# Performance work log

Hardware: AMD Instinct MI355X
Metric: run time of the kernel (lower is better)

Reference implementation:

```python
import jax, jax.numpy as jnp
import numpy as np

N = 100000   # nodes
E = 1600000  # edges
F = 128      # num_features
NF = 4       # n_factor
D = 64       # n_dim = dim // n_factor = 256 // 4
NL = 3       # n_layer
G = 128      # num graphs in batch


def setup_inputs() -> dict:
    key = jax.random.key(0)
    ks = jax.random.split(key, 10)
    s = 0.05
    x = jax.random.normal(ks[0], (N, F), jnp.float32)
    edge_index = jax.random.randint(ks[1], (2, E), 0, N)
    att = jax.random.uniform(ks[2], (NF, E), jnp.float32)
    batch = jnp.sort(jax.random.randint(ks[3], (N,), 0, G))
    lin_W = jax.random.normal(ks[4], (NF, F, D), jnp.float32) * s
    lin_b = jnp.zeros((NF, D), jnp.float32)
    conv_Wrel = jax.random.normal(ks[5], (NF, NL, D, D), jnp.float32) * s
    conv_brel = jnp.zeros((NF, NL, D), jnp.float32)
    conv_Wroot = jax.random.normal(ks[6], (NF, NL, D, D), jnp.float32) * s
    gru_Wih = jax.random.normal(ks[7], (NF, 3 * D, D), jnp.float32) * s
    gru_Whh = jax.random.normal(ks[8], (NF, 3 * D, D), jnp.float32) * s
    gru_bih = jnp.zeros((NF, 3 * D), jnp.float32)
    gru_bhh = jnp.zeros((NF, 3 * D), jnp.float32)
    return dict(x=x, edge_index=edge_index, att=att, batch=batch,
                lin_W=lin_W, lin_b=lin_b,
                conv_Wrel=conv_Wrel, conv_brel=conv_brel, conv_Wroot=conv_Wroot,
                gru_Wih=gru_Wih, gru_Whh=gru_Whh, gru_bih=gru_bih, gru_bhh=gru_bhh,
                num_graphs=G)


def _gru_cell(xin, h, Wih, Whh, bih, bhh):
    # torch.nn.GRU single step: r,z,n gates
    gi = xin @ Wih.T + bih  # [N, 3D]
    gh = h @ Whh.T + bhh
    ir, iz, inn = jnp.split(gi, 3, axis=-1)
    hr, hz, hn = jnp.split(gh, 3, axis=-1)
    r = jax.nn.sigmoid(ir + hr)
    z = jax.nn.sigmoid(iz + hz)
    n = jnp.tanh(inn + r * hn)
    return (1.0 - z) * n + z * h


def reference(x, edge_index, att, batch, lin_W, lin_b, conv_Wrel, conv_brel,
              conv_Wroot, gru_Wih, gru_Whh, gru_bih, gru_bhh, num_graphs):
    src, dst = edge_index[0], edge_index[1]
    counts = jax.ops.segment_sum(jnp.ones((N,), x.dtype), batch, num_segments=num_graphs)
    counts = jnp.maximum(counts, 1.0)[:, None]
    outs, feats = [], []
    for f in range(NF):
        w = att[f][:, None]                       # [E,1] edge weights for this factor
        out = x @ lin_W[f] + lin_b[f]             # [N,D]
        h = out                                   # initial GRU hidden state
        for l in range(NL):
            # GraphConv: lin_rel(scatter_add(w * x_src -> dst)) + lin_root(x)
            agg = jax.ops.segment_sum(out[src] * w, dst, num_segments=N)
            m = jax.nn.relu(agg @ conv_Wrel[f, l] + conv_brel[f, l] + out @ conv_Wroot[f, l])
            h = _gru_cell(m, h, gru_Wih[f], gru_Whh[f], gru_bih[f], gru_bhh[f])
            out = h
        feats.append(out)
        # global mean pool
        outs.append(jax.ops.segment_sum(out, batch, num_segments=num_graphs) / counts)
    return (jnp.stack(outs), jnp.stack(feats))
```

## Files before the change

kernel.cpp:

```cpp
#include <hip/hip_runtime.h>

#define NN   100000
#define EE   1600000
#define FDIM 128
#define NFAC 4
#define DD   64
#define NLAY 3
#define GG   128
#define ROW  (NFAC * DD)

#define PF_STRIDE 57344
#define OFF_WREL  8192
#define OFF_WROOT 20480
#define OFF_WIH   32768
#define OFF_WHH   45056
#define PREP_TOTAL (NFAC * PF_STRIDE)

typedef __bf16 bf16x8_t __attribute__((ext_vector_type(8)));
typedef float  f32x4_t  __attribute__((ext_vector_type(4)));

__device__ __forceinline__ unsigned short f2bf(float x) {
    unsigned u = __float_as_uint(x);
    u += 0x7fffu + ((u >> 16) & 1u);
    return (unsigned short)(u >> 16);
}
__device__ __forceinline__ float b2f(unsigned short h) {
    return __uint_as_float(((unsigned)h) << 16);
}
__device__ __forceinline__ float sigm(float x) { return 1.f / (1.f + __expf(-x)); }
__device__ __forceinline__ float tanh_f(float x) {
    float t = __expf(-2.f * fabsf(x));
    float r = (1.f - t) / (1.f + t);
    return x >= 0.f ? r : -r;
}

__global__ __launch_bounds__(256) void k_init(int* deg, int* cursor, float* outs) {
    int i = blockIdx.x * 256 + threadIdx.x;
    if (i < NN) { deg[i] = 0; cursor[i] = 0; }
    if (i < NFAC * GG * DD) outs[i] = 0.f;
}

__global__ __launch_bounds__(256) void k_prep(const float* x, const float* linW,
                                              const float* wrel, const float* wroot,
                                              const float* wih, const float* whh,
                                              unsigned short* x16, unsigned short* prep) {
    for (int i = blockIdx.x * 256 + threadIdx.x; i < NN * FDIM; i += gridDim.x * 256)
        x16[i] = f2bf(x[i]);
    for (int idx = blockIdx.x * 256 + threadIdx.x; idx < PREP_TOTAL; idx += gridDim.x * 256) {
        int f = idx / PF_STRIDE, r = idx % PF_STRIDE;
        int e, KB, mode, l = 0;
        if (r < OFF_WREL)       { e = r;                 KB = 4; mode = 0; }
        else if (r < OFF_WROOT) { int rr = r - OFF_WREL;  l = rr >> 12; e = rr & 4095; KB = 2; mode = 1; }
        else if (r < OFF_WIH)   { int rr = r - OFF_WROOT; l = rr >> 12; e = rr & 4095; KB = 2; mode = 2; }
        else if (r < OFF_WHH)   { e = r - OFF_WIH;        KB = 2; mode = 3; }
        else                    { e = r - OFF_WHH;        KB = 2; mode = 4; }
        int j = e & 7, lane = (e >> 3) & 63, t = e >> 9;
        int kb = t % KB, nt = t / KB;
        int k = kb * 32 + (lane >> 4) * 8 + j;
        int n = nt * 16 + (lane & 15);
        float v;
        if (mode == 0)      v = linW[(f * FDIM + k) * DD + n];
        else if (mode == 1) v = wrel[((f * 3 + l) * DD + k) * DD + n];
        else if (mode == 2) v = wroot[((f * 3 + l) * DD + k) * DD + n];
        else if (mode == 3) v = wih[(f * 192 + n) * DD + k];
        else                v = whh[(f * 192 + n) * DD + k];
        prep[idx] = f2bf(v);
    }
}

__global__ __launch_bounds__(256) void k_count(const int* batch, float* counts) {
    __shared__ int lb[GG + 1];
    int t = threadIdx.x;
    if (t <= GG) {
        int lo = 0, hi = NN;
        while (lo < hi) { int mid = (lo + hi) >> 1; if (batch[mid] < t) lo = mid + 1; else hi = mid; }
        lb[t] = lo;
    }
    __syncthreads();
    if (t < GG) counts[t] = (float)(lb[t + 1] - lb[t]);
}

__global__ __launch_bounds__(256) void k_deg(const int* ei, int* deg) {
    int e = blockIdx.x * 256 + threadIdx.x;
    if (e < EE) atomicAdd(&deg[ei[EE + e]], 1);
}
__global__ __launch_bounds__(256) void k_scan1(const int* deg, int* row_pos, int* bsum) {
    __shared__ int lds[256];
    int tid = threadIdx.x, idx = blockIdx.x * 256 + tid;
    int v = (idx < NN) ? deg[idx] : 0;
    lds[tid] = v; __syncthreads();
    for (int s = 1; s < 256; s <<= 1) {
        int t = (tid >= s) ? lds[tid - s] : 0;
        __syncthreads();
        lds[tid] += t;
        __syncthreads();
    }
    if (idx < NN) row_pos[idx] = lds[tid] - v;
    if (tid == 255) bsum[blockIdx.x] = lds[255];
}
__global__ __launch_bounds__(512) void k_scan2(int* bsum) {
    __shared__ int lds[512];
    int tid = threadIdx.x;
    int v = (tid < 391) ? bsum[tid] : 0;
    lds[tid] = v; __syncthreads();
    for (int s = 1; s < 512; s <<= 1) {
        int t = (tid >= s) ? lds[tid - s] : 0;
        __syncthreads();
        lds[tid] += t;
        __syncthreads();
    }
    bsum[tid] = lds[tid] - v;
}
__global__ __launch_bounds__(256) void k_rowptr(const int* row_pos, const int* boff, int* row_ptr) {
    int i = blockIdx.x * 256 + threadIdx.x;
    if (i < NN) row_ptr[i] = row_pos[i] + boff[i >> 8];
    if (i == 0) row_ptr[NN] = EE;
}
__global__ __launch_bounds__(256) void k_fill(const int* ei, const float* att,
                                              const int* row_ptr, int* cursor,
                                              int* csr_src, float* csr_att) {
    int e = blockIdx.x * 256 + threadIdx.x;
    if (e >= EE) return;
    int d = ei[EE + e];
    int slot = row_ptr[d] + atomicAdd(&cursor[d], 1);
    csr_src[slot] = ei[e];
    *(float4*)(csr_att + (size_t)slot * 4) =
        make_float4(att[e], att[EE + e], att[2 * EE + e], att[3 * EE + e]);
}

__global__ __launch_bounds__(256) void k_lin(const unsigned short* x16, const unsigned short* prep,
                                             const float* linb, unsigned short* out16) {
    int f = blockIdx.y, n0 = blockIdx.x * 64;
    __shared__ unsigned short xs[64 * 136];
    int tid = threadIdx.x;
    for (int t = tid; t < 1024; t += 256) {
        int row = t >> 4, seg = t & 15;
        int gn = n0 + row; if (gn >= NN) gn = NN - 1;
        *(uint4*)(xs + row * 136 + seg * 8) = *(const uint4*)(x16 + gn * FDIM + seg * 8);
    }
    __syncthreads();
    int w = tid >> 6, lane = tid & 63, mrow = lane & 15, q = lane >> 4;
    const unsigned short* wp = prep + f * PF_STRIDE;
#pragma unroll
    for (int nt = 0; nt < 4; nt++) {
        f32x4_t acc = {0.f, 0.f, 0.f, 0.f};
#pragma unroll
        for (int kb = 0; kb < 4; kb++) {
            bf16x8_t a = *(const bf16x8_t*)(xs + (w * 16 + mrow) * 136 + kb * 32 + q * 8);
            bf16x8_t b = *(const bf16x8_t*)(wp + ((nt * 4 + kb) * 64 + lane) * 8);
            acc = __builtin_amdgcn_mfma_f32_16x16x32_bf16(a, b, acc, 0, 0, 0);
        }
        int col = nt * 16 + mrow;
        float bias = linb[f * DD + col];
#pragma unroll
        for (int r = 0; r < 4; r++) {
            int node = n0 + w * 16 + q * 4 + r;
            if (node < NN) out16[(size_t)node * ROW + f * DD + col] = f2bf(acc[r] + bias);
        }
    }
}

__global__ __launch_bounds__(256) void k_gather(const int* row_ptr, const int* csr_src, const float* csr_att,
                                                const unsigned short* out16, unsigned short* agg16) {
    int wave = threadIdx.x >> 6, lane = threadIdx.x & 63;
    int n = blockIdx.x * 4 + wave;
    if (n >= NN) return;
    int row = row_ptr[n], end = row_ptr[n + 1];
    int total = end - row;
    int fsel = lane >> 4, loff = lane * 4;
    float a0 = 0.f, a1 = 0.f, a2 = 0.f, a3 = 0.f;
    for (int base = 0; base < total; base += 8) {
        int s[8]; float w[8];
#pragma unroll
        for (int j = 0; j < 8; j++) {
            int e = base + j;
            int idx = row + (e < total ? e : total - 1);
            s[j] = csr_src[idx];
            float ww = csr_att[(size_t)idx * 4 + fsel];
            w[j] = (e < total) ? ww : 0.f;
        }
        uint2 v[8];
#pragma unroll
        for (int j = 0; j < 8; j++)
            v[j] = *(const uint2*)(out16 + (size_t)s[j] * ROW + loff);
#pragma unroll
        for (int j = 0; j < 8; j++) {
            a0 = fmaf(w[j], __uint_as_float(v[j].x << 16), a0);
            a1 = fmaf(w[j], __uint_as_float(v[j].x & 0xffff0000u), a1);
            a2 = fmaf(w[j], __uint_as_float(v[j].y << 16), a2);
            a3 = fmaf(w[j], __uint_as_float(v[j].y & 0xffff0000u), a3);
        }
    }
    ushort4 r;
    r.x = f2bf(a0); r.y = f2bf(a1); r.z = f2bf(a2); r.w = f2bf(a3);
    *(ushort4*)(agg16 + (size_t)n * ROW + loff) = r;
}

__global__ __launch_bounds__(256) void k_layer(int l, const unsigned short* agg16, unsigned short* out16,
                                               const unsigned short* prep, const float* brel,
                                               const float* bih, const float* bhh,
                                               float* feats, int last) {
    int f = blockIdx.y, n0 = blockIdx.x * 64;
    __shared__ unsigned short A1[64 * 72];
    __shared__ unsigned short A2[64 * 72];
    __shared__ unsigned short Mt[64 * 72];
    int tid = threadIdx.x;
    for (int t = tid; t < 512; t += 256) {
        int row = t >> 3, seg = t & 7;
        int gn = n0 + row; if (gn >= NN) gn = NN - 1;
        *(uint4*)(A1 + row * 72 + seg * 8) = *(const uint4*)(agg16 + (size_t)gn * ROW + f * DD + seg * 8);
        *(uint4*)(A2 + row * 72 + seg * 8) = *(const uint4*)(out16 + (size_t)gn * ROW + f * DD + seg * 8);
    }
    __syncthreads();
    int w = tid >> 6, lane = tid & 63, mrow = lane & 15, q = lane >> 4;
    const unsigned short* wrel  = prep + f * PF_STRIDE + OFF_WREL  + l * 4096;
    const unsigned short* wroot = prep + f * PF_STRIDE + OFF_WROOT + l * 4096;

#pragma unroll
    for (int nt = 0; nt < 4; nt++) {
        f32x4_t acc = {0.f, 0.f, 0.f, 0.f};
#pragma unroll
        for (int kb = 0; kb < 2; kb++) {
            bf16x8_t a1 = *(const bf16x8_t*)(A1 + (w * 16 + mrow) * 72 + kb * 32 + q * 8);
            bf16x8_t b1 = *(const bf16x8_t*)(wrel + ((nt * 2 + kb) * 64 + lane) * 8);
            acc = __builtin_amdgcn_mfma_f32_16x16x32_bf16(a1, b1, acc, 0, 0, 0);
            bf16x8_t a2 = *(const bf16x8_t*)(A2 + (w * 16 + mrow) * 72 + kb * 32 + q * 8);
            bf16x8_t b2 = *(const bf16x8_t*)(wroot + ((nt * 2 + kb) * 64 + lane) * 8);
            acc = __builtin_amdgcn_mfma_f32_16x16x32_bf16(a2, b2, acc, 0, 0, 0);
        }
        int col = nt * 16 + mrow;
        float bias = brel[(f * 3 + l) * DD + col];
#pragma unroll
        for (int r = 0; r < 4; r++) {
            float mv = acc[r] + bias;
            mv = mv > 0.f ? mv : 0.f;
            Mt[(w * 16 + q * 4 + r) * 72 + col] = f2bf(mv);
        }
    }
    __syncthreads();

    const unsigned short* wih = prep + f * PF_STRIDE + OFF_WIH;
    const unsigned short* whh = prep + f * PF_STRIDE + OFF_WHH;
#pragma unroll
    for (int nt = 0; nt < 4; nt++) {
        f32x4_t ir = {0.f,0.f,0.f,0.f}, iz = {0.f,0.f,0.f,0.f}, in_ = {0.f,0.f,0.f,0.f};
        f32x4_t hr = {0.f,0.f,0.f,0.f}, hz = {0.f,0.f,0.f,0.f}, hn  = {0.f,0.f,0.f,0.f};
#pragma unroll
        for (int kb = 0; kb < 2; kb++) {
            bf16x8_t am = *(const bf16x8_t*)(Mt + (w * 16 + mrow) * 72 + kb * 32 + q * 8);
            bf16x8_t ah = *(const bf16x8_t*)(A2 + (w * 16 + mrow) * 72 + kb * 32 + q * 8);
            bf16x8_t br = *(const bf16x8_t*)(wih + (((nt)     * 2 + kb) * 64 + lane) * 8);
            bf16x8_t bz = *(const bf16x8_t*)(wih + (((nt + 4) * 2 + kb) * 64 + lane) * 8);
            bf16x8_t bn = *(const bf16x8_t*)(wih + (((nt + 8) * 2 + kb) * 64 + lane) * 8);
            ir = __builtin_amdgcn_mfma_f32_16x16x32_bf16(am, br, ir, 0, 0, 0);
            iz = __builtin_amdgcn_mfma_f32_16x16x32_bf16(am, bz, iz, 0, 0, 0);
            in_ = __builtin_amdgcn_mfma_f32_16x16x32_bf16(am, bn, in_, 0, 0, 0);
            bf16x8_t cr = *(const bf16x8_t*)(whh + (((nt)     * 2 + kb) * 64 + lane) * 8);
            bf16x8_t cz = *(const bf16x8_t*)(whh + (((nt + 4) * 2 + kb) * 64 + lane) * 8);
            bf16x8_t cn = *(const bf16x8_t*)(whh + (((nt + 8) * 2 + kb) * 64 + lane) * 8);
            hr = __builtin_amdgcn_mfma_f32_16x16x32_bf16(ah, cr, hr, 0, 0, 0);
            hz = __builtin_amdgcn_mfma_f32_16x16x32_bf16(ah, cz, hz, 0, 0, 0);
            hn = __builtin_amdgcn_mfma_f32_16x16x32_bf16(ah, cn, hn, 0, 0, 0);
        }
        int col = nt * 16 + mrow;
        float bi_r = bih[f * 192 + col],        bh_r = bhh[f * 192 + col];
        float bi_z = bih[f * 192 + 64 + col],   bh_z = bhh[f * 192 + 64 + col];
        float bi_n = bih[f * 192 + 128 + col],  bh_n = bhh[f * 192 + 128 + col];
#pragma unroll
        for (int r = 0; r < 4; r++) {
            float rg = sigm(ir[r] + bi_r + hr[r] + bh_r);
            float z  = sigm(iz[r] + bi_z + hz[r] + bh_z);
            float nn = tanh_f(in_[r] + bi_n + rg * (hn[r] + bh_n));
            float h  = b2f(A2[(w * 16 + q * 4 + r) * 72 + col]);
            float hp = (1.f - z) * nn + z * h;
            int node = n0 + w * 16 + q * 4 + r;
            if (node < NN) {
                out16[(size_t)node * ROW + f * DD + col] = f2bf(hp);
                if (last) feats[((size_t)f * NN + node) * DD + col] = hp;
            }
        }
    }
}

__global__ __launch_bounds__(256) void k_pool(const float* feats, const int* batch, float* outs) {
    int f = blockIdx.y, w = threadIdx.x >> 6, lane = threadIdx.x & 63;
    int nbase = blockIdx.x * 256 + w * 64;
    if (nbase >= NN) return;
    int g_cur = batch[nbase];
    float acc = 0.f;
    for (int i = 0; i < 64; i++) {
        int n = nbase + i;
        if (n >= NN) break;
        int g = batch[n];
        float v = feats[((size_t)f * NN + n) * DD + lane];
        if (g != g_cur) {
            atomicAdd(&outs[(f * GG + g_cur) * DD + lane], acc);
            acc = v; g_cur = g;
        } else acc += v;
    }
    atomicAdd(&outs[(f * GG + g_cur) * DD + lane], acc);
}
__global__ __launch_bounds__(256) void k_norm(float* outs, const float* counts) {
    int i = blockIdx.x * 256 + threadIdx.x;
    if (i < NFAC * GG * DD) {
        int g = (i >> 6) & (GG - 1);
        outs[i] /= fmaxf(counts[g], 1.f);
    }
}

extern "C" void kernel_launch(void* const* d_in, const int* in_sizes, int n_in,
                              void* d_out, int out_size, void* d_ws, size_t ws_size,
                              hipStream_t stream) {
    const float* x    = (const float*)d_in[0];
    const int*   ei   = (const int*)d_in[1];
    const float* att  = (const float*)d_in[2];
    const int*   batch= (const int*)d_in[3];
    const float* linW = (const float*)d_in[4];
    const float* linb = (const float*)d_in[5];
    const float* wrel = (const float*)d_in[6];
    const float* brel = (const float*)d_in[7];
    const float* wroot= (const float*)d_in[8];
    const float* wih  = (const float*)d_in[9];
    const float* whh  = (const float*)d_in[10];
    const float* bih  = (const float*)d_in[11];
    const float* bhh  = (const float*)d_in[12];

    float* outs  = (float*)d_out;
    float* feats = (float*)d_out + NFAC * GG * DD;

    char* p = (char*)d_ws;
    unsigned short* out16 = (unsigned short*)p; p += (size_t)NN * ROW * 2;
    unsigned short* agg16 = (unsigned short*)p; p += (size_t)NN * ROW * 2;
    unsigned short* x16   = (unsigned short*)p; p += (size_t)NN * FDIM * 2;
    unsigned short* prep  = (unsigned short*)p; p += (size_t)PREP_TOTAL * 2;
    float* csr_att        = (float*)p;          p += (size_t)EE * 16;
    int* csr_src          = (int*)p;            p += (size_t)EE * 4;
    int* deg              = (int*)p;            p += (size_t)NN * 4;
    int* cursor           = (int*)p;            p += (size_t)NN * 4;
    int* row_pos          = (int*)p;            p += (size_t)NN * 4;
    int* row_ptr          = (int*)p;            p += (size_t)(NN + 1) * 4;
    int* boff             = (int*)p;            p += 512 * 4;
    float* counts         = (float*)p;          p += 512;

    k_init  <<<dim3(391),  dim3(256), 0, stream>>>(deg, cursor, outs);
    k_prep  <<<dim3(4096), dim3(256), 0, stream>>>(x, linW, wrel, wroot, wih, whh, x16, prep);
    k_count <<<dim3(1),    dim3(256), 0, stream>>>(batch, counts);
    k_deg   <<<dim3(6250), dim3(256), 0, stream>>>(ei, deg);
    k_scan1 <<<dim3(391),  dim3(256), 0, stream>>>(deg, row_pos, boff);
    k_scan2 <<<dim3(1),    dim3(512), 0, stream>>>(boff);
    k_rowptr<<<dim3(391),  dim3(256), 0, stream>>>(row_pos, boff, row_ptr);
    k_fill  <<<dim3(6250), dim3(256), 0, stream>>>(ei, att, row_ptr, cursor, csr_src, csr_att);
    k_lin   <<<dim3(1563, 4), dim3(256), 0, stream>>>(x16, prep, linb, out16);
    for (int l = 0; l < NLAY; l++) {
        k_gather<<<dim3(25000),   dim3(256), 0, stream>>>(row_ptr, csr_src, csr_att, out16, agg16);
        k_layer <<<dim3(1563, 4), dim3(256), 0, stream>>>(l, agg16, out16, prep, brel, bih, bhh,
                                                          feats, (l == NLAY - 1) ? 1 : 0);
    }
    k_pool <<<dim3(391, 4), dim3(256), 0, stream>>>(feats, batch, outs);
    k_norm <<<dim3(128),    dim3(256), 0, stream>>>(outs, counts);
}
```

Baseline: 1.050 ms.

## Fuse edge gather with conv+GRU layer kernel and ping-pong hidden buffers

The separate gather and layer kernels are merged into one kernel per layer. Each 64-node block gathers neighbor aggregates for all four factors into shared memory and then runs the conv and GRU MFMAs, with one wave assigned per factor. This removes the agg16 round trip through global memory and one launch per layer, and double-buffers the hidden state so the in-place update is not read by other blocks mid-layer. In exchange, the gather now has much less parallelism (1563 blocks with 16 serial nodes per wave instead of 25000 blocks), and the larger shared-memory footprint limits occupancy, which may expose latency.

```diff
diff --git a/kernel.cpp b/kernel.cpp
--- a/kernel.cpp
+++ b/kernel.cpp
@@ -15,6 +15,8 @@
 #define OFF_WIH   32768
 #define OFF_WHH   45056
 #define PREP_TOTAL (NFAC * PF_STRIDE)
+
+#define LPAD 264
 
 typedef __bf16 bf16x8_t __attribute__((ext_vector_type(8)));
 typedef float  f32x4_t  __attribute__((ext_vector_type(4)));
@@ -130,153 +132,180 @@
 
 __global__ __launch_bounds__(256) void k_lin(const unsigned short* x16, const unsigned short* prep,
                                              const float* linb, unsigned short* out16) {
-    int f = blockIdx.y, n0 = blockIdx.x * 64;
+    int n0 = blockIdx.x * 64;
     __shared__ unsigned short xs[64 * 136];
     int tid = threadIdx.x;
     for (int t = tid; t < 1024; t += 256) {
         int row = t >> 4, seg = t & 15;
         int gn = n0 + row; if (gn >= NN) gn = NN - 1;
-        *(uint4*)(xs + row * 136 + seg * 8) = *(const uint4*)(x16 + gn * FDIM + seg * 8);
+        *(uint4*)(xs + row * 136 + seg * 8) = *(const uint4*)(x16 + (size_t)gn * FDIM + seg * 8);
     }
     __syncthreads();
     int w = tid >> 6, lane = tid & 63, mrow = lane & 15, q = lane >> 4;
-    const unsigned short* wp = prep + f * PF_STRIDE;
-#pragma unroll
-    for (int nt = 0; nt < 4; nt++) {
-        f32x4_t acc = {0.f, 0.f, 0.f, 0.f};
-#pragma unroll
-        for (int kb = 0; kb < 4; kb++) {
-            bf16x8_t a = *(const bf16x8_t*)(xs + (w * 16 + mrow) * 136 + kb * 32 + q * 8);
-            bf16x8_t b = *(const bf16x8_t*)(wp + ((nt * 4 + kb) * 64 + lane) * 8);
-            acc = __builtin_amdgcn_mfma_f32_16x16x32_bf16(a, b, acc, 0, 0, 0);
-        }
-        int col = nt * 16 + mrow;
-        float bias = linb[f * DD + col];
-#pragma unroll
-        for (int r = 0; r < 4; r++) {
-            int node = n0 + w * 16 + q * 4 + r;
-            if (node < NN) out16[(size_t)node * ROW + f * DD + col] = f2bf(acc[r] + bias);
-        }
-    }
-}
-
-__global__ __launch_bounds__(256) void k_gather(const int* row_ptr, const int* csr_src, const float* csr_att,
-                                                const unsigned short* out16, unsigned short* agg16) {
-    int wave = threadIdx.x >> 6, lane = threadIdx.x & 63;
-    int n = blockIdx.x * 4 + wave;
-    if (n >= NN) return;
-    int row = row_ptr[n], end = row_ptr[n + 1];
-    int total = end - row;
+    const unsigned short* wp = prep + w * PF_STRIDE;
+    for (int mt = 0; mt < 4; mt++) {
+        bf16x8_t a[4];
+#pragma unroll
+        for (int kb = 0; kb < 4; kb++)
+            a[kb] = *(const bf16x8_t*)(xs + (mt * 16 + mrow) * 136 + kb * 32 + q * 8);
+#pragma unroll
+        for (int nt = 0; nt < 4; nt++) {
+            f32x4_t acc = {0.f, 0.f, 0.f, 0.f};
+#pragma unroll
+            for (int kb = 0; kb < 4; kb++) {
+                bf16x8_t b = *(const bf16x8_t*)(wp + ((nt * 4 + kb) * 64 + lane) * 8);
+                acc = __builtin_amdgcn_mfma_f32_16x16x32_bf16(a[kb], b, acc, 0, 0, 0);
+            }
+            int col = nt * 16 + mrow;
+            float bias = linb[w * DD + col];
+#pragma unroll
+            for (int r = 0; r < 4; r++) {
+                int node = n0 + mt * 16 + q * 4 + r;
+                if (node < NN) out16[(size_t)node * ROW + w * DD + col] = f2bf(acc[r] + bias);
+            }
+        }
+    }
+}
+
+__global__ __launch_bounds__(256, 2) void k_fused(int l,
+        const int* row_ptr, const int* csr_src, const float* csr_att,
+        const unsigned short* in16, unsigned short* out16,
+        const unsigned short* prep, const float* brel,
+        const float* bih, const float* bhh, float* feats, int last)
+{
+    int n0 = blockIdx.x * 64;
+    __shared__ unsigned short A1[64 * LPAD];
+    __shared__ unsigned short A2[64 * LPAD];
+    int tid = threadIdx.x;
+    int w = tid >> 6, lane = tid & 63;
+
+    uint4 hreg[8];
+#pragma unroll
+    for (int t = 0; t < 8; t++) {
+        int idx = tid + t * 256;
+        int row = idx >> 5, seg = idx & 31;
+        int gn = n0 + row; if (gn >= NN) gn = NN - 1;
+        hreg[t] = *(const uint4*)(in16 + (size_t)gn * ROW + seg * 8);
+    }
+
     int fsel = lane >> 4, loff = lane * 4;
-    float a0 = 0.f, a1 = 0.f, a2 = 0.f, a3 = 0.f;
-    for (int base = 0; base < total; base += 8) {
-        int s[8]; float w[8];
-#pragma unroll
-        for (int j = 0; j < 8; j++) {
-            int e = base + j;
-            int idx = row + (e < total ? e : total - 1);
-            s[j] = csr_src[idx];
-            float ww = csr_att[(size_t)idx * 4 + fsel];
-            w[j] = (e < total) ? ww : 0.f;
-        }
-        uint2 v[8];
-#pragma unroll
-        for (int j = 0; j < 8; j++)
-            v[j] = *(const uint2*)(out16 + (size_t)s[j] * ROW + loff);
-#pragma unroll
-        for (int j = 0; j < 8; j++) {
-            a0 = fmaf(w[j], __uint_as_float(v[j].x << 16), a0);
-            a1 = fmaf(w[j], __uint_as_float(v[j].x & 0xffff0000u), a1);
-            a2 = fmaf(w[j], __uint_as_float(v[j].y << 16), a2);
-            a3 = fmaf(w[j], __uint_as_float(v[j].y & 0xffff0000u), a3);
-        }
-    }
-    ushort4 r;
-    r.x = f2bf(a0); r.y = f2bf(a1); r.z = f2bf(a2); r.w = f2bf(a3);
-    *(ushort4*)(agg16 + (size_t)n * ROW + loff) = r;
-}
-
-__global__ __launch_bounds__(256) void k_layer(int l, const unsigned short* agg16, unsigned short* out16,
-                                               const unsigned short* prep, const float* brel,
-                                               const float* bih, const float* bhh,
-                                               float* feats, int last) {
-    int f = blockIdx.y, n0 = blockIdx.x * 64;
-    __shared__ unsigned short A1[64 * 72];
-    __shared__ unsigned short A2[64 * 72];
-    __shared__ unsigned short Mt[64 * 72];
-    int tid = threadIdx.x;
-    for (int t = tid; t < 512; t += 256) {
-        int row = t >> 3, seg = t & 7;
-        int gn = n0 + row; if (gn >= NN) gn = NN - 1;
-        *(uint4*)(A1 + row * 72 + seg * 8) = *(const uint4*)(agg16 + (size_t)gn * ROW + f * DD + seg * 8);
-        *(uint4*)(A2 + row * 72 + seg * 8) = *(const uint4*)(out16 + (size_t)gn * ROW + f * DD + seg * 8);
+    for (int i = 0; i < 16; i++) {
+        int li = w * 16 + i;
+        int n = n0 + li; if (n >= NN) n = NN - 1;
+        int row = row_ptr[n], end = row_ptr[n + 1];
+        int total = end - row;
+        float g0 = 0.f, g1 = 0.f, g2 = 0.f, g3 = 0.f;
+        for (int base = 0; base < total; base += 8) {
+            int s_[8]; float wt[8];
+#pragma unroll
+            for (int j = 0; j < 8; j++) {
+                int e = base + j;
+                int idx = row + (e < total ? e : total - 1);
+                s_[j] = csr_src[idx];
+                float ww = csr_att[(size_t)idx * 4 + fsel];
+                wt[j] = (e < total) ? ww : 0.f;
+            }
+            uint2 v[8];
+#pragma unroll
+            for (int j = 0; j < 8; j++)
+                v[j] = *(const uint2*)(in16 + (size_t)s_[j] * ROW + loff);
+#pragma unroll
+            for (int j = 0; j < 8; j++) {
+                g0 = fmaf(wt[j], __uint_as_float(v[j].x << 16), g0);
+                g1 = fmaf(wt[j], __uint_as_float(v[j].x & 0xffff0000u), g1);
+                g2 = fmaf(wt[j], __uint_as_float(v[j].y << 16), g2);
+                g3 = fmaf(wt[j], __uint_as_float(v[j].y & 0xffff0000u), g3);
+            }
+        }
+        ushort4 rr;
+        rr.x = f2bf(g0); rr.y = f2bf(g1); rr.z = f2bf(g2); rr.w = f2bf(g3);
+        *(ushort4*)(A1 + li * LPAD + loff) = rr;
+    }
+
+#pragma unroll
+    for (int t = 0; t < 8; t++) {
+        int idx = tid + t * 256;
+        int row = idx >> 5, seg = idx & 31;
+        *(uint4*)(A2 + row * LPAD + seg * 8) = hreg[t];
     }
     __syncthreads();
-    int w = tid >> 6, lane = tid & 63, mrow = lane & 15, q = lane >> 4;
-    const unsigned short* wrel  = prep + f * PF_STRIDE + OFF_WREL  + l * 4096;
-    const unsigned short* wroot = prep + f * PF_STRIDE + OFF_WROOT + l * 4096;
-
-#pragma unroll
-    for (int nt = 0; nt < 4; nt++) {
-        f32x4_t acc = {0.f, 0.f, 0.f, 0.f};
+
+    int mrow = lane & 15, q = lane >> 4;
+    const unsigned short* wrel  = prep + w * PF_STRIDE + OFF_WREL  + l * 4096;
+    const unsigned short* wroot = prep + w * PF_STRIDE + OFF_WROOT + l * 4096;
+
+    for (int mt = 0; mt < 4; mt++) {
+        bf16x8_t a1f[2], a2f[2];
 #pragma unroll
         for (int kb = 0; kb < 2; kb++) {
-            bf16x8_t a1 = *(const bf16x8_t*)(A1 + (w * 16 + mrow) * 72 + kb * 32 + q * 8);
-            bf16x8_t b1 = *(const bf16x8_t*)(wrel + ((nt * 2 + kb) * 64 + lane) * 8);
-            acc = __builtin_amdgcn_mfma_f32_16x16x32_bf16(a1, b1, acc, 0, 0, 0);
-            bf16x8_t a2 = *(const bf16x8_t*)(A2 + (w * 16 + mrow) * 72 + kb * 32 + q * 8);
-            bf16x8_t b2 = *(const bf16x8_t*)(wroot + ((nt * 2 + kb) * 64 + lane) * 8);
-            acc = __builtin_amdgcn_mfma_f32_16x16x32_bf16(a2, b2, acc, 0, 0, 0);
-        }
-        int col = nt * 16 + mrow;
-        float bias = brel[(f * 3 + l) * DD + col];
-#pragma unroll
-        for (int r = 0; r < 4; r++) {
-            float mv = acc[r] + bias;
-            mv = mv > 0.f ? mv : 0.f;
-            Mt[(w * 16 + q * 4 + r) * 72 + col] = f2bf(mv);
-        }
-    }
-    __syncthreads();
-
-    const unsigned short* wih = prep + f * PF_STRIDE + OFF_WIH;
-    const unsigned short* whh = prep + f * PF_STRIDE + OFF_WHH;
-#pragma unroll
-    for (int nt = 0; nt < 4; nt++) {
-        f32x4_t ir = {0.f,0.f,0.f,0.f}, iz = {0.f,0.f,0.f,0.f}, in_ = {0.f,0.f,0.f,0.f};
-        f32x4_t hr = {0.f,0.f,0.f,0.f}, hz = {0.f,0.f,0.f,0.f}, hn  = {0.f,0.f,0.f,0.f};
+            a1f[kb] = *(const bf16x8_t*)(A1 + (mt * 16 + mrow) * LPAD + w * DD + kb * 32 + q * 8);
+            a2f[kb] = *(const bf16x8_t*)(A2 + (mt * 16 + mrow) * LPAD + w * DD + kb * 32 + q * 8);
+        }
+#pragma unroll
+        for (int nt = 0; nt < 4; nt++) {
+            f32x4_t acc = {0.f, 0.f, 0.f, 0.f};
+#pragma unroll
+            for (int kb = 0; kb < 2; kb++) {
+                bf16x8_t b1 = *(const bf16x8_t*)(wrel + ((nt * 2 + kb) * 64 + lane) * 8);
+                acc = __builtin_amdgcn_mfma_f32_16x16x32_bf16(a1f[kb], b1, acc, 0, 0, 0);
+                bf16x8_t b2 = *(const bf16x8_t*)(wroot + ((nt * 2 + kb) * 64 + lane) * 8);
+                acc = __builtin_amdgcn_mfma_f32_16x16x32_bf16(a2f[kb], b2, acc, 0, 0, 0);
+            }
+            int col = nt * 16 + mrow;
+            float bias = brel[(w * 3 + l) * DD + col];
+#pragma unroll
+            for (int r = 0; r < 4; r++) {
+                float mv = acc[r] + bias;
+                mv = mv > 0.f ? mv : 0.f;
+                A1[(mt * 16 + q * 4 + r) * LPAD + w * DD + col] = f2bf(mv);
+            }
+        }
+    }
+
+    const unsigned short* wih = prep + w * PF_STRIDE + OFF_WIH;
+    const unsigned short* whh = prep + w * PF_STRIDE + OFF_WHH;
+    for (int mt = 0; mt < 4; mt++) {
+        bf16x8_t amf[2], ahf[2];
 #pragma unroll
         for (int kb = 0; kb < 2; kb++) {
-            bf16x8_t am = *(const bf16x8_t*)(Mt + (w * 16 + mrow) * 72 + kb * 32 + q * 8);
-            bf16x8_t ah = *(const bf16x8_t*)(A2 + (w * 16 + mrow) * 72 + kb * 32 + q * 8);
-            bf16x8_t br = *(const bf16x8_t*)(wih + (((nt)     * 2 + kb) * 64 + lane) * 8);
-            bf16x8_t bz = *(const bf16x8_t*)(wih + (((nt + 4) * 2 + kb) * 64 + lane) * 8);
-            bf16x8_t bn = *(const bf16x8_t*)(wih + (((nt + 8) * 2 + kb) * 64 + lane) * 8);
-            ir = __builtin_amdgcn_mfma_f32_16x16x32_bf16(am, br, ir, 0, 0, 0);
-            iz = __builtin_amdgcn_mfma_f32_16x16x32_bf16(am, bz, iz, 0, 0, 0);
-            in_ = __builtin_amdgcn_mfma_f32_16x16x32_bf16(am, bn, in_, 0, 0, 0);
-            bf16x8_t cr = *(const bf16x8_t*)(whh + (((nt)     * 2 + kb) * 64 + lane) * 8);
-            bf16x8_t cz = *(const bf16x8_t*)(whh + (((nt + 4) * 2 + kb) * 64 + lane) * 8);
-            bf16x8_t cn = *(const bf16x8_t*)(whh + (((nt + 8) * 2 + kb) * 64 + lane) * 8);
-            hr = __builtin_amdgcn_mfma_f32_16x16x32_bf16(ah, cr, hr, 0, 0, 0);
-            hz = __builtin_amdgcn_mfma_f32_16x16x32_bf16(ah, cz, hz, 0, 0, 0);
-            hn = __builtin_amdgcn_mfma_f32_16x16x32_bf16(ah, cn, hn, 0, 0, 0);
-        }
-        int col = nt * 16 + mrow;
-        float bi_r = bih[f * 192 + col],        bh_r = bhh[f * 192 + col];
-        float bi_z = bih[f * 192 + 64 + col],   bh_z = bhh[f * 192 + 64 + col];
-        float bi_n = bih[f * 192 + 128 + col],  bh_n = bhh[f * 192 + 128 + col];
-#pragma unroll
-        for (int r = 0; r < 4; r++) {
-            float rg = sigm(ir[r] + bi_r + hr[r] + bh_r);
-            float z  = sigm(iz[r] + bi_z + hz[r] + bh_z);
-            float nn = tanh_f(in_[r] + bi_n + rg * (hn[r] + bh_n));
-            float h  = b2f(A2[(w * 16 + q * 4 + r) * 72 + col]);
-            float hp = (1.f - z) * nn + z * h;
-            int node = n0 + w * 16 + q * 4 + r;
-            if (node < NN) {
-                out16[(size_t)node * ROW + f * DD + col] = f2bf(hp);
-                if (last) feats[((size_t)f * NN + node) * DD + col] = hp;
+            amf[kb] = *(const bf16x8_t*)(A1 + (mt * 16 + mrow) * LPAD + w * DD + kb * 32 + q * 8);
+            ahf[kb] = *(const bf16x8_t*)(A2 + (mt * 16 + mrow) * LPAD + w * DD + kb * 32 + q * 8);
+        }
+#pragma unroll
+        for (int nt = 0; nt < 4; nt++) {
+            f32x4_t ir = {0.f,0.f,0.f,0.f}, iz = {0.f,0.f,0.f,0.f}, in_ = {0.f,0.f,0.f,0.f};
+            f32x4_t hr = {0.f,0.f,0.f,0.f}, hz = {0.f,0.f,0.f,0.f}, hn  = {0.f,0.f,0.f,0.f};
+#pragma unroll
+            for (int kb = 0; kb < 2; kb++) {
+                bf16x8_t br = *(const bf16x8_t*)(wih + (((nt)     * 2 + kb) * 64 + lane) * 8);
+                bf16x8_t bz = *(const bf16x8_t*)(wih + (((nt + 4) * 2 + kb) * 64 + lane) * 8);
+                bf16x8_t bn = *(const bf16x8_t*)(wih + (((nt + 8) * 2 + kb) * 64 + lane) * 8);
+                ir  = __builtin_amdgcn_mfma_f32_16x16x32_bf16(amf[kb], br, ir, 0, 0, 0);
+                iz  = __builtin_amdgcn_mfma_f32_16x16x32_bf16(amf[kb], bz, iz, 0, 0, 0);
+                in_ = __builtin_amdgcn_mfma_f32_16x16x32_bf16(amf[kb], bn, in_, 0, 0, 0);
+                bf16x8_t cr = *(const bf16x8_t*)(whh + (((nt)     * 2 + kb) * 64 + lane) * 8);
+                bf16x8_t cz = *(const bf16x8_t*)(whh + (((nt + 4) * 2 + kb) * 64 + lane) * 8);
+                bf16x8_t cn = *(const bf16x8_t*)(whh + (((nt + 8) * 2 + kb) * 64 + lane) * 8);
+                hr = __builtin_amdgcn_mfma_f32_16x16x32_bf16(ahf[kb], cr, hr, 0, 0, 0);
+                hz = __builtin_amdgcn_mfma_f32_16x16x32_bf16(ahf[kb], cz, hz, 0, 0, 0);
+                hn = __builtin_amdgcn_mfma_f32_16x16x32_bf16(ahf[kb], cn, hn, 0, 0, 0);
+            }
+            int col = nt * 16 + mrow;
+            float bi_r = bih[w * 192 + col],        bh_r = bhh[w * 192 + col];
+            float bi_z = bih[w * 192 + 64 + col],   bh_z = bhh[w * 192 + 64 + col];
+            float bi_n = bih[w * 192 + 128 + col],  bh_n = bhh[w * 192 + 128 + col];
+#pragma unroll
+            for (int r = 0; r < 4; r++) {
+                float rg = sigm(ir[r] + bi_r + hr[r] + bh_r);
+                float z  = sigm(iz[r] + bi_z + hz[r] + bh_z);
+                float nn = tanh_f(in_[r] + bi_n + rg * (hn[r] + bh_n));
+                float h  = b2f(A2[(mt * 16 + q * 4 + r) * LPAD + w * DD + col]);
+                float hp = (1.f - z) * nn + z * h;
+                int node = n0 + mt * 16 + q * 4 + r;
+                if (node < NN) {
+                    out16[(size_t)node * ROW + w * DD + col] = f2bf(hp);
+                    if (last) feats[((size_t)w * NN + node) * DD + col] = hp;
+                }
             }
         }
     }
@@ -329,8 +358,8 @@
     float* feats = (float*)d_out + NFAC * GG * DD;
 
     char* p = (char*)d_ws;
-    unsigned short* out16 = (unsigned short*)p; p += (size_t)NN * ROW * 2;
-    unsigned short* agg16 = (unsigned short*)p; p += (size_t)NN * ROW * 2;
+    unsigned short* bufA  = (unsigned short*)p; p += (size_t)NN * ROW * 2;
+    unsigned short* bufB  = (unsigned short*)p; p += (size_t)NN * ROW * 2;
     unsigned short* x16   = (unsigned short*)p; p += (size_t)NN * FDIM * 2;
     unsigned short* prep  = (unsigned short*)p; p += (size_t)PREP_TOTAL * 2;
     float* csr_att        = (float*)p;          p += (size_t)EE * 16;
@@ -350,11 +379,13 @@
     k_scan2 <<<dim3(1),    dim3(512), 0, stream>>>(boff);
     k_rowptr<<<dim3(391),  dim3(256), 0, stream>>>(row_pos, boff, row_ptr);
     k_fill  <<<dim3(6250), dim3(256), 0, stream>>>(ei, att, row_ptr, cursor, csr_src, csr_att);
-    k_lin   <<<dim3(1563, 4), dim3(256), 0, stream>>>(x16, prep, linb, out16);
+    k_lin   <<<dim3(1563), dim3(256), 0, stream>>>(x16, prep, linb, bufA);
+    unsigned short* bufs[2] = { bufA, bufB };
     for (int l = 0; l < NLAY; l++) {
-        k_gather<<<dim3(25000),   dim3(256), 0, stream>>>(row_ptr, csr_src, csr_att, out16, agg16);
-        k_layer <<<dim3(1563, 4), dim3(256), 0, stream>>>(l, agg16, out16, prep, brel, bih, bhh,
-                                                          feats, (l == NLAY - 1) ? 1 : 0);
+        k_fused<<<dim3(1563), dim3(256), 0, stream>>>(l, row_ptr, csr_src, csr_att,
+                                                      bufs[l & 1], bufs[(l + 1) & 1],
+                                                      prep, brel, bih, bhh,
+                                                      feats, (l == NLAY - 1) ? 1 : 0);
     }
     k_pool <<<dim3(391, 4), dim3(256), 0, stream>>>(feats, batch, outs);
     k_norm <<<dim3(128),    dim3(256), 0, stream>>>(outs, counts);
```

Result: slower. 1.258 ms (+19.7%).
